# Performance work log

Measured on AMD Instinct MI355X. Metric: run time of the kernel, lower is better.

The kernel has to match this reference:

```python
import jax, jax.numpy as jnp
import numpy as np

EPS = 1e-5

def _patches(x, k, stride, pad):
    # x: [B, C, H, W] -> [B, L, C*k*k] with patch features ordered (c, kh, kw)
    # matching torch unfold / adder2d weight layout [Cout, Cin, kh, kw].
    B, C, H, W = x.shape
    xp = jnp.pad(x, ((0, 0), (0, 0), (pad, pad), (pad, pad)))
    Ho = (H + 2 * pad - k) // stride + 1
    Wo = (W + 2 * pad - k) // stride + 1
    cols = [xp[:, :, i:i + stride * Ho:stride, j:j + stride * Wo:stride]
            for i in range(k) for j in range(k)]
    p = jnp.stack(cols, axis=2)                      # [B, C, k*k, Ho, Wo]
    p = p.reshape(B, C * k * k, Ho * Wo)             # [B, K, L]
    return p.transpose(0, 2, 1), Ho, Wo              # [B, L, K]


def adder2d(x, w, stride, pad):
    # AdderNet layer: out[n,co,h,w] = -sum_{ci,kh,kw} |x_patch - w[co]|
    B = x.shape[0]
    Cout, Cin, k, _ = w.shape
    P, Ho, Wo = _patches(x, k, stride, pad)          # [B, L, K]
    Wf = w.reshape(Cout, Cin * k * k)                # [Cout, K]

    @jax.checkpoint
    def per_out(wrow):                               # wrow: [K]
        return -jnp.sum(jnp.abs(P - wrow), axis=-1)  # [B, L]

    out = jax.lax.map(per_out, Wf)                   # [Cout, B, L]
    return out.transpose(1, 0, 2).reshape(B, Cout, Ho, Wo)


def batchnorm(x, gamma, beta):
    # training-mode BatchNorm2d: batch statistics over (N, H, W)
    mu = jnp.mean(x, axis=(0, 2, 3), keepdims=True)
    var = jnp.var(x, axis=(0, 2, 3), keepdims=True)
    xn = (x - mu) * jax.lax.rsqrt(var + EPS)
    return xn * gamma[None, :, None, None] + beta[None, :, None, None]


def setup_inputs() -> dict:
    key = jax.random.key(0)
    kx, kw1, kw2 = jax.random.split(key, 3)
    B, C, H, W = 32, 64, 32, 32
    return {
        "x": jax.random.normal(kx, (B, C, H, W), dtype=jnp.float32),
        "w1": jax.random.normal(kw1, (C, C, 3, 3), dtype=jnp.float32),
        "g1": jnp.ones((C,), dtype=jnp.float32),
        "b1": jnp.zeros((C,), dtype=jnp.float32),
        "w2": jax.random.normal(kw2, (C, C, 3, 3), dtype=jnp.float32),
        "g2": jnp.ones((C,), dtype=jnp.float32),
        "b2": jnp.zeros((C,), dtype=jnp.float32),
    }


def reference(x, w1, g1, b1, w2, g2, b2):
    out = adder2d(x, w1, stride=1, pad=1)
    out = jax.nn.relu(batchnorm(out, g1, b1))
    out = adder2d(out, w2, stride=1, pad=1)
    out = batchnorm(out, g2, b2)
    return jax.nn.relu(out + x)
```

## Files before the change

### kernel.cpp

```cpp
#include <hip/hip_runtime.h>

#define CH    64
#define HWHW  1024
#define CHW   65536
#define NPIX  32768.0f
#define KDIM  576

#define QSCALE 524288.0f
#define QBIAS  4194304.5f
#define Q0     4194304u
#define QINV   1.9073486328125e-6f

__device__ __forceinline__ unsigned quantf(float x) {
  return (unsigned)fmaf(x, QSCALE, QBIAS);
}

__device__ __forceinline__ unsigned sad_acc(unsigned x, unsigned w, unsigned a) {
  unsigned d;
  asm("v_sad_u32 %0, %1, %2, %3" : "=v"(d) : "v"(x), "v"(w), "v"(a));
  return d;
}

__global__ __launch_bounds__(256) void prep_kernel(
    const float* __restrict__ w1, const float* __restrict__ w2,
    unsigned* __restrict__ wt1, unsigned* __restrict__ wt2,
    float* __restrict__ stats) {
  int i = blockIdx.x * 256 + threadIdx.x;
  if (i < 256) stats[i] = 0.0f;
  if (i < CH * KDIM) {
    int co = i / KDIM, k = i % KDIM;
    int dst = (co >> 2) * 2304 + k * 4 + (co & 3);
    wt1[dst] = quantf(w1[i]);
    wt2[dst] = quantf(w2[i]);
  }
}

__global__ __launch_bounds__(256, 6) void adder_kernel(
    const float* __restrict__ xin,
    const unsigned* __restrict__ wt,
    float* __restrict__ out,
    float* __restrict__ stats) {
  const int cog  = blockIdx.x;
  const int rg   = blockIdx.y;
  const int n    = blockIdx.z;
  const int tid  = threadIdx.x;
  const int lane = tid & 63;
  const int wv   = __builtin_amdgcn_readfirstlane(tid >> 6);
  const int co0  = cog * 4;
  const int r0   = lane >> 3;
  const int c0   = (lane & 7) * 4;

  __shared__ __align__(16) unsigned lds[3840];
  unsigned* xsw = lds + wv * 360;
  unsigned* wl  = lds + 1440;
  unsigned* red = lds;

  const int rowA = lane >> 3, c4A = lane & 7;
  const int hrA  = rg * 8 - 1 + rowA;
  const bool vA  = (hrA >= 0) && (hrA < 32);
  const int rowB = (lane + 64) >> 3, c4B = lane & 7;
  const int hrB  = rg * 8 - 1 + rowB;
  const bool vB  = (lane < 16) && (hrB >= 0) && (hrB < 32);
  const float* gbase = xin + n * CHW + (wv * 16) * HWHW;
  const float* gA = gbase + hrA * 32 + c4A * 4;
  const float* gB = gbase + hrB * 32 + c4B * 4;
  unsigned* dA = xsw + rowA * 36 + c4A * 4;
  unsigned* dB = xsw + rowB * 36 + c4B * 4;

  float4 a0, a1;
  if (vA) a0 = *(const float4*)gA;
  if (vB) a1 = *(const float4*)gB;
  {
    const uint4* wsrc = (const uint4*)(wt + cog * 2304);
    for (int i = tid; i < 576; i += 256) ((uint4*)wl)[i] = wsrc[i];
  }
  for (int i = lane; i < 360; i += 64) xsw[i] = Q0;
  __syncthreads();
  if (vA) { uint4 q = {quantf(a0.x), quantf(a0.y), quantf(a0.z), quantf(a0.w)}; *(uint4*)dA = q; }
  if (vB) { uint4 q = {quantf(a1.x), quantf(a1.y), quantf(a1.z), quantf(a1.w)}; *(uint4*)dB = q; }

  unsigned acc[4][4];
#pragma unroll
  for (int co = 0; co < 4; ++co)
#pragma unroll
    for (int j = 0; j < 4; ++j) acc[co][j] = 0u;

  const int off0 = c0 ? (c0 - 1) : 33;

  for (int ci = 0; ci < 16; ++ci) {
    const bool more = ci < 15;
    float4 b0, b1;
    if (more && vA) b0 = *(const float4*)(gA + (ci + 1) * HWHW);
    if (more && vB) b1 = *(const float4*)(gB + (ci + 1) * HWHW);

    const int ph = wv * 48 + ci * 3;
#pragma unroll
    for (int kh = 0; kh < 3; ++kh) {
      const uint4* wp = (const uint4*)(wl + (ph + kh) * 12);
      uint4 wa = wp[0], wb = wp[1], wc = wp[2];
      unsigned w[12] = {wa.x, wa.y, wa.z, wa.w, wb.x, wb.y, wb.z, wb.w,
                        wc.x, wc.y, wc.z, wc.w};
      const unsigned* rp = xsw + (r0 + kh) * 36;
      uint4 x4 = *(const uint4*)(rp + c0);
      unsigned xl = rp[off0];
      unsigned xr = rp[c0 + 4];
      unsigned xv[6] = {xl, x4.x, x4.y, x4.z, x4.w, xr};
#pragma unroll
      for (int kw = 0; kw < 3; ++kw)
#pragma unroll
        for (int co = 0; co < 4; ++co) {
          unsigned ww = w[kw * 4 + co];
          acc[co][0] = sad_acc(xv[kw + 0], ww, acc[co][0]);
          acc[co][1] = sad_acc(xv[kw + 1], ww, acc[co][1]);
          acc[co][2] = sad_acc(xv[kw + 2], ww, acc[co][2]);
          acc[co][3] = sad_acc(xv[kw + 3], ww, acc[co][3]);
        }
    }
    __builtin_amdgcn_wave_barrier();
    if (more && vA) { uint4 q = {quantf(b0.x), quantf(b0.y), quantf(b0.z), quantf(b0.w)}; *(uint4*)dA = q; }
    if (more && vB) { uint4 q = {quantf(b1.x), quantf(b1.y), quantf(b1.z), quantf(b1.w)}; *(uint4*)dB = q; }
    __builtin_amdgcn_wave_barrier();
  }

  __syncthreads();
  if (wv != 0) {
    unsigned* rp = red + (wv - 1) * 1280 + lane * 20;
#pragma unroll
    for (int co = 0; co < 4; ++co) {
      uint4 q = {acc[co][0], acc[co][1], acc[co][2], acc[co][3]};
      *(uint4*)(rp + co * 4) = q;
    }
  }
  __syncthreads();

  if (wv == 0) {
#pragma unroll
    for (int s = 0; s < 3; ++s) {
      const unsigned* rp = red + s * 1280 + lane * 20;
#pragma unroll
      for (int co = 0; co < 4; ++co) {
        uint4 q = *(const uint4*)(rp + co * 4);
        acc[co][0] += q.x; acc[co][1] += q.y; acc[co][2] += q.z; acc[co][3] += q.w;
      }
    }
    const int ob = n * CHW + (rg * 8 + r0) * 32 + c0;
#pragma unroll
    for (int co = 0; co < 4; ++co) {
      float t0 = -(float)acc[co][0] * QINV;
      float t1 = -(float)acc[co][1] * QINV;
      float t2 = -(float)acc[co][2] * QINV;
      float t3 = -(float)acc[co][3] * QINV;
      *(float4*)(out + ob + (co0 + co) * HWHW) = make_float4(t0, t1, t2, t3);
      float sm = t0 + t1 + t2 + t3;
      float sq = t0 * t0 + t1 * t1 + t2 * t2 + t3 * t3;
#pragma unroll
      for (int m = 1; m < 64; m <<= 1) {
        sm += __shfl_xor(sm, m);
        sq += __shfl_xor(sq, m);
      }
      if (lane == 0) {
        atomicAdd(stats + co0 + co, sm);
        atomicAdd(stats + 64 + co0 + co, sq);
      }
    }
  }
}

__global__ __launch_bounds__(256) void bnrelu_kernel(
    const float* __restrict__ A, const float* __restrict__ stats,
    const float* __restrict__ g, const float* __restrict__ b,
    float* __restrict__ B) {
  int i = blockIdx.x * 256 + threadIdx.x;
  int c = (i >> 8) & 63;
  float mu  = stats[c] * (1.0f / NPIX);
  float var = fmaf(-mu, mu, stats[64 + c] * (1.0f / NPIX));
  float rs  = rsqrtf(var + 1e-5f);
  float ga  = g[c] * rs;
  float be  = fmaf(-mu, ga, b[c]);
  float4 v = ((const float4*)A)[i];
  v.x = fmaxf(fmaf(v.x, ga, be), 0.0f);
  v.y = fmaxf(fmaf(v.y, ga, be), 0.0f);
  v.z = fmaxf(fmaf(v.z, ga, be), 0.0f);
  v.w = fmaxf(fmaf(v.w, ga, be), 0.0f);
  ((float4*)B)[i] = v;
}

__global__ __launch_bounds__(256) void final_kernel(
    const float* __restrict__ Cbuf, const float* __restrict__ stats,
    const float* __restrict__ g, const float* __restrict__ b,
    const float* __restrict__ xres, float* __restrict__ out) {
  int i = blockIdx.x * 256 + threadIdx.x;
  int c = (i >> 8) & 63;
  float mu  = stats[c] * (1.0f / NPIX);
  float var = fmaf(-mu, mu, stats[64 + c] * (1.0f / NPIX));
  float rs  = rsqrtf(var + 1e-5f);
  float ga  = g[c] * rs;
  float be  = fmaf(-mu, ga, b[c]);
  float4 v = ((const float4*)Cbuf)[i];
  float4 xr = ((const float4*)xres)[i];
  v.x = fmaxf(fmaf(v.x, ga, be) + xr.x, 0.0f);
  v.y = fmaxf(fmaf(v.y, ga, be) + xr.y, 0.0f);
  v.z = fmaxf(fmaf(v.z, ga, be) + xr.z, 0.0f);
  v.w = fmaxf(fmaf(v.w, ga, be) + xr.w, 0.0f);
  ((float4*)out)[i] = v;
}

extern "C" void kernel_launch(void* const* d_in, const int* in_sizes, int n_in,
                              void* d_out, int out_size, void* d_ws, size_t ws_size,
                              hipStream_t stream) {
  const float* x  = (const float*)d_in[0];
  const float* w1 = (const float*)d_in[1];
  const float* g1 = (const float*)d_in[2];
  const float* b1 = (const float*)d_in[3];
  const float* w2 = (const float*)d_in[4];
  const float* g2 = (const float*)d_in[5];
  const float* b2 = (const float*)d_in[6];
  float* outp = (float*)d_out;

  float* ws = (float*)d_ws;
  const size_t NEL = 2097152;
  float*    bufA  = ws;
  float*    bufB  = ws + NEL;
  unsigned* wt1   = (unsigned*)(ws + 2 * NEL);
  unsigned* wt2   = wt1 + CH * KDIM;
  float*    stats = (float*)(wt2 + CH * KDIM);

  prep_kernel<<<144, 256, 0, stream>>>(w1, w2, wt1, wt2, stats);

  dim3 agrid(16, 4, 32);
  adder_kernel<<<agrid, 256, 0, stream>>>(x, wt1, bufA, stats);
  bnrelu_kernel<<<2048, 256, 0, stream>>>(bufA, stats, g1, b1, bufB);
  adder_kernel<<<agrid, 256, 0, stream>>>(bufB, wt2, bufA, stats + 128);
  final_kernel<<<2048, 256, 0, stream>>>(bufA, stats + 128, g2, b2, x, outp);
}
```

Baseline: 157.5 us.

## Pack two channels as 16-bit and use v_sad_u16 for paired SAD

Quantizes activations and weights to 16-bit with clamping and packs two input channels into each 32-bit word. One v_sad_u16 then accumulates absolute differences for both channels, halving the SAD instruction count and the LDS traffic per channel. The LDS row stride becomes 37 with a one-word left pad, which removes the separate left-halo load. Coarser quantization (scale 4096, clamped to 16 bits) loses precision and saturates large values, so accuracy may fall outside tolerance, especially for the second layer's post-ReLU inputs.

```diff
diff --git a/kernel.cpp b/kernel.cpp
--- a/kernel.cpp
+++ b/kernel.cpp
@@ -4,20 +4,23 @@
 #define HWHW  1024
 #define CHW   65536
 #define NPIX  32768.0f
-#define KDIM  576
-
-#define QSCALE 524288.0f
-#define QBIAS  4194304.5f
-#define Q0     4194304u
-#define QINV   1.9073486328125e-6f
-
-__device__ __forceinline__ unsigned quantf(float x) {
-  return (unsigned)fmaf(x, QSCALE, QBIAS);
-}
-
-__device__ __forceinline__ unsigned sad_acc(unsigned x, unsigned w, unsigned a) {
+
+#define QS16   4096.0f
+#define QB16   32768.5f
+#define Q0P    0x80008000u
+#define QINV16 2.44140625e-4f
+
+__device__ __forceinline__ unsigned q16(float x) {
+  unsigned u = (unsigned)fmaf(x, QS16, QB16);
+  return u > 65535u ? 65535u : u;
+}
+__device__ __forceinline__ unsigned q16pk(float lo, float hi) {
+  return q16(lo) | (q16(hi) << 16);
+}
+
+__device__ __forceinline__ unsigned sad16(unsigned x, unsigned w, unsigned a) {
   unsigned d;
-  asm("v_sad_u32 %0, %1, %2, %3" : "=v"(d) : "v"(x), "v"(w), "v"(a));
+  asm("v_sad_u16 %0, %1, %2, %3" : "=v"(d) : "v"(x), "v"(w), "v"(a));
   return d;
 }
 
@@ -25,13 +28,20 @@
     const float* __restrict__ w1, const float* __restrict__ w2,
     unsigned* __restrict__ wt1, unsigned* __restrict__ wt2,
     float* __restrict__ stats) {
-  int i = blockIdx.x * 256 + threadIdx.x;
-  if (i < 256) stats[i] = 0.0f;
-  if (i < CH * KDIM) {
-    int co = i / KDIM, k = i % KDIM;
-    int dst = (co >> 2) * 2304 + k * 4 + (co & 3);
-    wt1[dst] = quantf(w1[i]);
-    wt2[dst] = quantf(w2[i]);
+  int j = blockIdx.x * 256 + threadIdx.x;
+  if (j < 256) stats[j] = 0.0f;
+  if (j < 18432) {
+    int colo = j & 3;
+    int t = j >> 2;
+    int kw = t % 3; t /= 3;
+    int kh = t % 3; t /= 3;
+    int cp = t & 7; t >>= 3;
+    int wv = t & 3; int cog = t >> 2;
+    int co  = cog * 4 + colo;
+    int cil = wv * 16 + cp * 2;
+    int slo = co * 576 + cil * 9 + kh * 3 + kw;
+    wt1[j] = q16pk(w1[slo], w1[slo + 9]);
+    wt2[j] = q16pk(w2[slo], w2[slo + 9]);
   }
 }
 
@@ -51,33 +61,35 @@
   const int c0   = (lane & 7) * 4;
 
   __shared__ __align__(16) unsigned lds[3840];
-  unsigned* xsw = lds + wv * 360;
-  unsigned* wl  = lds + 1440;
+  unsigned* xsw = lds + wv * 370;
+  unsigned* wl  = lds + 1480;
   unsigned* red = lds;
 
   const int rowA = lane >> 3, c4A = lane & 7;
   const int hrA  = rg * 8 - 1 + rowA;
   const bool vA  = (hrA >= 0) && (hrA < 32);
-  const int rowB = (lane + 64) >> 3, c4B = lane & 7;
+  const int rowB = (lane + 64) >> 3;
   const int hrB  = rg * 8 - 1 + rowB;
   const bool vB  = (lane < 16) && (hrB >= 0) && (hrB < 32);
   const float* gbase = xin + n * CHW + (wv * 16) * HWHW;
   const float* gA = gbase + hrA * 32 + c4A * 4;
-  const float* gB = gbase + hrB * 32 + c4B * 4;
-  unsigned* dA = xsw + rowA * 36 + c4A * 4;
-  unsigned* dB = xsw + rowB * 36 + c4B * 4;
-
-  float4 a0, a1;
-  if (vA) a0 = *(const float4*)gA;
-  if (vB) a1 = *(const float4*)gB;
+  const float* gB = gbase + hrB * 32 + c4A * 4;
+  unsigned* dA = xsw + rowA * 37 + 1 + c4A * 4;
+  unsigned* dB = xsw + rowB * 37 + 1 + c4A * 4;
+
+  float4 a0, a1, b0, b1;
+  if (vA) { a0 = *(const float4*)gA; a1 = *(const float4*)(gA + HWHW); }
+  if (vB) { b0 = *(const float4*)gB; b1 = *(const float4*)(gB + HWHW); }
   {
-    const uint4* wsrc = (const uint4*)(wt + cog * 2304);
-    for (int i = tid; i < 576; i += 256) ((uint4*)wl)[i] = wsrc[i];
-  }
-  for (int i = lane; i < 360; i += 64) xsw[i] = Q0;
+    const uint4* wsrc = (const uint4*)(wt + cog * 1152);
+    for (int i = tid; i < 288; i += 256) ((uint4*)wl)[i] = wsrc[i];
+  }
+  for (int i = lane; i < 370; i += 64) xsw[i] = Q0P;
   __syncthreads();
-  if (vA) { uint4 q = {quantf(a0.x), quantf(a0.y), quantf(a0.z), quantf(a0.w)}; *(uint4*)dA = q; }
-  if (vB) { uint4 q = {quantf(a1.x), quantf(a1.y), quantf(a1.z), quantf(a1.w)}; *(uint4*)dB = q; }
+  if (vA) { dA[0] = q16pk(a0.x, a1.x); dA[1] = q16pk(a0.y, a1.y);
+            dA[2] = q16pk(a0.z, a1.z); dA[3] = q16pk(a0.w, a1.w); }
+  if (vB) { dB[0] = q16pk(b0.x, b1.x); dB[1] = q16pk(b0.y, b1.y);
+            dB[2] = q16pk(b0.z, b1.z); dB[3] = q16pk(b0.w, b1.w); }
 
   unsigned acc[4][4];
 #pragma unroll
@@ -85,40 +97,41 @@
 #pragma unroll
     for (int j = 0; j < 4; ++j) acc[co][j] = 0u;
 
-  const int off0 = c0 ? (c0 - 1) : 33;
-
-  for (int ci = 0; ci < 16; ++ci) {
-    const bool more = ci < 15;
-    float4 b0, b1;
-    if (more && vA) b0 = *(const float4*)(gA + (ci + 1) * HWHW);
-    if (more && vB) b1 = *(const float4*)(gB + (ci + 1) * HWHW);
-
-    const int ph = wv * 48 + ci * 3;
+  for (int cp = 0; cp < 8; ++cp) {
+    const bool more = cp < 7;
+    float4 pa0, pa1, pb0, pb1;
+    if (more && vA) { pa0 = *(const float4*)(gA + (2 * cp + 2) * HWHW);
+                      pa1 = *(const float4*)(gA + (2 * cp + 3) * HWHW); }
+    if (more && vB) { pb0 = *(const float4*)(gB + (2 * cp + 2) * HWHW);
+                      pb1 = *(const float4*)(gB + (2 * cp + 3) * HWHW); }
+
+    const unsigned* wpb = wl + wv * 288 + cp * 36;
 #pragma unroll
     for (int kh = 0; kh < 3; ++kh) {
-      const uint4* wp = (const uint4*)(wl + (ph + kh) * 12);
+      const uint4* wp = (const uint4*)(wpb + kh * 12);
       uint4 wa = wp[0], wb = wp[1], wc = wp[2];
       unsigned w[12] = {wa.x, wa.y, wa.z, wa.w, wb.x, wb.y, wb.z, wb.w,
                         wc.x, wc.y, wc.z, wc.w};
-      const unsigned* rp = xsw + (r0 + kh) * 36;
-      uint4 x4 = *(const uint4*)(rp + c0);
-      unsigned xl = rp[off0];
-      unsigned xr = rp[c0 + 4];
-      unsigned xv[6] = {xl, x4.x, x4.y, x4.z, x4.w, xr};
+      const unsigned* rp = xsw + (r0 + kh) * 37 + c0;
+      unsigned xv[6];
+#pragma unroll
+      for (int j = 0; j < 6; ++j) xv[j] = rp[j];
 #pragma unroll
       for (int kw = 0; kw < 3; ++kw)
 #pragma unroll
         for (int co = 0; co < 4; ++co) {
           unsigned ww = w[kw * 4 + co];
-          acc[co][0] = sad_acc(xv[kw + 0], ww, acc[co][0]);
-          acc[co][1] = sad_acc(xv[kw + 1], ww, acc[co][1]);
-          acc[co][2] = sad_acc(xv[kw + 2], ww, acc[co][2]);
-          acc[co][3] = sad_acc(xv[kw + 3], ww, acc[co][3]);
+          acc[co][0] = sad16(xv[kw + 0], ww, acc[co][0]);
+          acc[co][1] = sad16(xv[kw + 1], ww, acc[co][1]);
+          acc[co][2] = sad16(xv[kw + 2], ww, acc[co][2]);
+          acc[co][3] = sad16(xv[kw + 3], ww, acc[co][3]);
         }
     }
     __builtin_amdgcn_wave_barrier();
-    if (more && vA) { uint4 q = {quantf(b0.x), quantf(b0.y), quantf(b0.z), quantf(b0.w)}; *(uint4*)dA = q; }
-    if (more && vB) { uint4 q = {quantf(b1.x), quantf(b1.y), quantf(b1.z), quantf(b1.w)}; *(uint4*)dB = q; }
+    if (more && vA) { dA[0] = q16pk(pa0.x, pa1.x); dA[1] = q16pk(pa0.y, pa1.y);
+                      dA[2] = q16pk(pa0.z, pa1.z); dA[3] = q16pk(pa0.w, pa1.w); }
+    if (more && vB) { dB[0] = q16pk(pb0.x, pb1.x); dB[1] = q16pk(pb0.y, pb1.y);
+                      dB[2] = q16pk(pb0.z, pb1.z); dB[3] = q16pk(pb0.w, pb1.w); }
     __builtin_amdgcn_wave_barrier();
   }
 
@@ -146,10 +159,10 @@
     const int ob = n * CHW + (rg * 8 + r0) * 32 + c0;
 #pragma unroll
     for (int co = 0; co < 4; ++co) {
-      float t0 = -(float)acc[co][0] * QINV;
-      float t1 = -(float)acc[co][1] * QINV;
-      float t2 = -(float)acc[co][2] * QINV;
-      float t3 = -(float)acc[co][3] * QINV;
+      float t0 = -(float)acc[co][0] * QINV16;
+      float t1 = -(float)acc[co][1] * QINV16;
+      float t2 = -(float)acc[co][2] * QINV16;
+      float t3 = -(float)acc[co][3] * QINV16;
       *(float4*)(out + ob + (co0 + co) * HWHW) = make_float4(t0, t1, t2, t3);
       float sm = t0 + t1 + t2 + t3;
       float sq = t0 * t0 + t1 * t1 + t2 * t2 + t3 * t3;
@@ -222,10 +235,10 @@
   float*    bufA  = ws;
   float*    bufB  = ws + NEL;
   unsigned* wt1   = (unsigned*)(ws + 2 * NEL);
-  unsigned* wt2   = wt1 + CH * KDIM;
-  float*    stats = (float*)(wt2 + CH * KDIM);
-
-  prep_kernel<<<144, 256, 0, stream>>>(w1, w2, wt1, wt2, stats);
+  unsigned* wt2   = wt1 + 18432;
+  float*    stats = (float*)(wt2 + 18432);
+
+  prep_kernel<<<72, 256, 0, stream>>>(w1, w2, wt1, wt2, stats);
 
   dim3 agrid(16, 4, 32);
   adder_kernel<<<agrid, 256, 0, stream>>>(x, wt1, bufA, stats);
```

Measured after the change: 145.1 us. 7.9% less time.
